# Kernel optimization log

Measured on AMD Instinct MI355X. Metric: run time of the kernel, lower is better.

## Reference

```python
import jax, jax.numpy as jnp
import numpy as np

B, S, HID = 1, 2048, 4096
N_HEADS, N_KV_HEADS, HEAD_DIM = 32, 8, 128
ROPE_THETA = 10000.0


def rotate_half(x):
    # standard Llama rotate_half along last dim
    d = x.shape[-1] // 2
    return jnp.concatenate([-x[..., d:], x[..., :d]], axis=-1)


def rope_cos_sin(position_ids, dtype):
    # inv_freq: [head_dim/2]
    inv_freq = 1.0 / (ROPE_THETA ** (jnp.arange(0, HEAD_DIM, 2, dtype=jnp.float32) / HEAD_DIM))
    freqs = position_ids.astype(jnp.float32)[:, :, None] * inv_freq[None, None, :]  # [B,S,hd/2]
    emb = jnp.concatenate([freqs, freqs], axis=-1)  # [B,S,hd]
    return jnp.cos(emb).astype(dtype), jnp.sin(emb).astype(dtype)


def setup_inputs() -> dict:
    key = jax.random.key(0)
    ks = jax.random.split(key, 5)
    scale = 0.02
    return {
        "hidden_states": jax.random.normal(ks[0], (B, S, HID), dtype=jnp.float32),
        "position_ids": jnp.broadcast_to(jnp.arange(S, dtype=jnp.int32)[None, :], (B, S)),
        "Wq": jax.random.normal(ks[1], (N_HEADS * HEAD_DIM, HID), dtype=jnp.float32) * scale,
        "Wk": jax.random.normal(ks[2], (N_KV_HEADS * HEAD_DIM, HID), dtype=jnp.float32) * scale,
        "Wv": jax.random.normal(ks[3], (N_KV_HEADS * HEAD_DIM, HID), dtype=jnp.float32) * scale,
        "Wo": jax.random.normal(ks[4], (HID, HID), dtype=jnp.float32) * scale,
    }


def reference(hidden_states, position_ids, Wq, Wk, Wv, Wo):
    bsz, q_len, _ = hidden_states.shape
    n_rep = N_HEADS // N_KV_HEADS

    # projections (torch Linear: x @ W.T)
    q = (hidden_states @ Wq.T).reshape(bsz, q_len, N_HEADS, HEAD_DIM).transpose(0, 2, 1, 3)
    k = (hidden_states @ Wk.T).reshape(bsz, q_len, N_KV_HEADS, HEAD_DIM).transpose(0, 2, 1, 3)
    v = (hidden_states @ Wv.T).reshape(bsz, q_len, N_KV_HEADS, HEAD_DIM).transpose(0, 2, 1, 3)

    cos, sin = rope_cos_sin(position_ids, hidden_states.dtype)
    cos = cos[:, None, :, :]  # [B,1,S,hd]
    sin = sin[:, None, :, :]
    q = q * cos + rotate_half(q) * sin
    k = k * cos + rotate_half(k) * sin

    # GQA: repeat kv heads
    k = jnp.repeat(k, n_rep, axis=1)  # [B,nH,S,hd]
    v = jnp.repeat(v, n_rep, axis=1)

    scores = jnp.einsum("bhqd,bhkd->bhqk", q, k) / jnp.sqrt(jnp.asarray(HEAD_DIM, q.dtype))
    causal = jnp.tril(jnp.ones((q_len, q_len), dtype=bool))
    neg = jnp.asarray(jnp.finfo(jnp.float32).min, scores.dtype)
    scores = jnp.where(causal[None, None, :, :], scores, neg)

    attn = jax.nn.softmax(scores.astype(jnp.float32), axis=-1).astype(q.dtype)
    out = jnp.einsum("bhqk,bhkd->bhqd", attn, v)  # [B,nH,S,hd]
    out = out.transpose(0, 2, 1, 3).reshape(bsz, q_len, HID)
    return out @ Wo.T
```

## Files before the change

### kernel.cpp

```cpp
#include <hip/hip_runtime.h>

typedef __attribute__((ext_vector_type(4))) float f32x4;
typedef __attribute__((ext_vector_type(8))) __bf16 bf16x8;
typedef __attribute__((ext_vector_type(4))) unsigned short u16x4;

#define DEVI static __device__ __forceinline__
#define AS1 __attribute__((address_space(1)))
#define AS3 __attribute__((address_space(3)))

static constexpr int S_LEN = 2048;
static constexpr int HID   = 4096;
static constexpr int NH    = 32;
static constexpr int NKV   = 8;
static constexpr int HD    = 128;
static constexpr int NQKV  = HID + 2 * NKV * HD;

DEVI unsigned short f2bf(float f) {
  unsigned int u = __float_as_uint(f);
  u += 0x7FFFu + ((u >> 16) & 1u);
  return (unsigned short)(u >> 16);
}
DEVI float bf2f(unsigned short h) {
  return __uint_as_float(((unsigned int)h) << 16);
}

__global__ void cast_f32_bf16(const float* __restrict__ in,
                              unsigned short* __restrict__ out, int n4) {
  int i = blockIdx.x * 256 + threadIdx.x;
  if (i >= n4) return;
  float4 v = reinterpret_cast<const float4*>(in)[i];
  u16x4 o;
  o[0] = f2bf(v.x); o[1] = f2bf(v.y); o[2] = f2bf(v.z); o[3] = f2bf(v.w);
  reinterpret_cast<u16x4*>(out)[i] = o;
}

__global__ void rope_table(float2* __restrict__ tab) {
  int i = blockIdx.x * 256 + threadIdx.x;
  if (i >= S_LEN * 64) return;
  int j = i & 63, s = i >> 6;
  float inv = powf(10000.0f, -(float)j / 64.0f);
  float ang = (float)s * inv;
  tab[i] = make_float2(cosf(ang), sinf(ang));
}

__global__ void rope_all(unsigned short* __restrict__ Qb,
                         unsigned short* __restrict__ Kb,
                         const float2* __restrict__ tab) {
  const int totq = S_LEN * NH * 64;
  const int tot  = totq + S_LEN * NKV * 64;
  int i = blockIdx.x * 256 + threadIdx.x;
  if (i >= tot) return;
  unsigned short* X; int Hn, idx;
  if (i < totq) { X = Qb; Hn = NH; idx = i; }
  else          { X = Kb; Hn = NKV; idx = i - totq; }
  int j = idx & 63;
  int h = (idx >> 6) % Hn;
  int s = idx / (64 * Hn);
  float2 cs = tab[s * 64 + j];
  unsigned short* p = X + (size_t)s * Hn * HD + h * HD;
  float x1 = bf2f(p[j]);
  float x2 = bf2f(p[j + 64]);
  p[j]      = f2bf(x1 * cs.x - x2 * cs.y);
  p[j + 64] = f2bf(x2 * cs.x + x1 * cs.y);
}

__global__ __launch_bounds__(512, 4) void gemm_qkv192(
    const unsigned short* __restrict__ A,
    const unsigned short* __restrict__ B,
    unsigned short* __restrict__ Qb,
    unsigned short* __restrict__ Kb,
    unsigned short* __restrict__ Vt) {
  __shared__ __align__(16) unsigned short lds[2][20480];
  const int tid = threadIdx.x;
  const int lane = tid & 63, w = tid >> 6;
  const int wm = w >> 2, wn = w & 3;
  const int lr = lane & 15, lg = lane >> 4;
  const int n0 = blockIdx.x * 192, m0 = blockIdx.y * 128;
  const int Kd = HID;

  const int sAr = tid >> 3, sAp = tid & 7;
  auto stA = [&](int buf, int t, int u) {
    int row = u * 64 + sAr;
    __builtin_amdgcn_global_load_lds(
        (const AS1 void*)(A + (size_t)(m0 + row) * Kd + t * 64 + ((sAp ^ (row & 7)) * 8)),
        (AS3 void*)(&lds[buf][row * 64 + sAp * 8]), 16, 0, 0);
  };
  auto stB = [&](int buf, int t, int v) {
    int row = v * 64 + sAr;
    __builtin_amdgcn_global_load_lds(
        (const AS1 void*)(B + (size_t)(n0 + row) * Kd + t * 64 + ((sAp ^ (row & 7)) * 8)),
        (AS3 void*)(&lds[buf][8192 + row * 64 + sAp * 8]), 16, 0, 0);
  };

  const int arow = (wm * 64 + lr) * 64;
  const int brow = 8192 + (wn * 48 + lr) * 64;
  const int ck0 = ((lg) ^ (lr & 7)) * 8;
  const int ck1 = ((4 + lg) ^ (lr & 7)) * 8;

  f32x4 acc[4][3] = {};
  bf16x8 bgr[3];

#pragma unroll
  for (int u = 0; u < 2; ++u) { stA(0, 0, u); stA(1, 1, u); }
#pragma unroll
  for (int v = 0; v < 3; ++v) { stB(0, 0, v); stB(1, 1, v); }
  asm volatile("s_waitcnt vmcnt(0)" ::: "memory");
  __builtin_amdgcn_s_barrier();

#define QPHASE(BUF, KH, MH, LOADB, WAITOP, ...)                                \
  do {                                                                         \
    const int ck = (KH) ? ck1 : ck0;                                           \
    const unsigned short* ab = &lds[BUF][arow + (MH) * 2048 + ck];             \
    bf16x8 af0 = *reinterpret_cast<const bf16x8*>(ab);                         \
    bf16x8 af1 = *reinterpret_cast<const bf16x8*>(ab + 1024);                  \
    if (LOADB) {                                                               \
      const unsigned short* bb = &lds[BUF][brow + ck];                         \
      bgr[0] = *reinterpret_cast<const bf16x8*>(bb);                           \
      bgr[1] = *reinterpret_cast<const bf16x8*>(bb + 1024);                    \
      bgr[2] = *reinterpret_cast<const bf16x8*>(bb + 2048);                    \
    }                                                                          \
    __builtin_amdgcn_sched_barrier(0);                                         \
    __VA_ARGS__                                                                \
    WAITOP                                                                     \
    __builtin_amdgcn_s_barrier();                                              \
    asm volatile("s_waitcnt lgkmcnt(0)" ::: "memory");                         \
    __builtin_amdgcn_sched_barrier(0);                                         \
    __builtin_amdgcn_s_setprio(1);                                             \
    acc[(MH)*2+0][0] = __builtin_amdgcn_mfma_f32_16x16x32_bf16(af0, bgr[0], acc[(MH)*2+0][0],0,0,0); \
    acc[(MH)*2+0][1] = __builtin_amdgcn_mfma_f32_16x16x32_bf16(af0, bgr[1], acc[(MH)*2+0][1],0,0,0); \
    acc[(MH)*2+0][2] = __builtin_amdgcn_mfma_f32_16x16x32_bf16(af0, bgr[2], acc[(MH)*2+0][2],0,0,0); \
    acc[(MH)*2+1][0] = __builtin_amdgcn_mfma_f32_16x16x32_bf16(af1, bgr[0], acc[(MH)*2+1][0],0,0,0); \
    acc[(MH)*2+1][1] = __builtin_amdgcn_mfma_f32_16x16x32_bf16(af1, bgr[1], acc[(MH)*2+1][1],0,0,0); \
    acc[(MH)*2+1][2] = __builtin_amdgcn_mfma_f32_16x16x32_bf16(af1, bgr[2], acc[(MH)*2+1][2],0,0,0); \
    __builtin_amdgcn_s_setprio(0);                                             \
    __builtin_amdgcn_s_barrier();                                              \
  } while (0)

#define QVM0 asm volatile("s_waitcnt vmcnt(0)" ::: "memory");
#define QNOW

  for (int i = 0; i < 32; ++i) {
    const int t = 2 * i;
    const bool nf = (i != 0), nl = (i != 31);
    QPHASE(0, 0, 0, 1, QNOW, if (nf) { stA(1, t + 1, 0); stA(1, t + 1, 1);
                                       stB(1, t + 1, 0); stB(1, t + 1, 1); stB(1, t + 1, 2); });
    QPHASE(0, 0, 1, 0, QNOW, ;);
    QPHASE(0, 1, 0, 1, QNOW, ;);
    QPHASE(0, 1, 1, 0, QVM0, ;);
    QPHASE(1, 0, 0, 1, QNOW, if (nl) { stA(0, t + 2, 0); stA(0, t + 2, 1);
                                       stB(0, t + 2, 0); stB(0, t + 2, 1); stB(0, t + 2, 2); });
    QPHASE(1, 0, 1, 0, QNOW, ;);
    QPHASE(1, 1, 0, 1, QNOW, ;);
    QPHASE(1, 1, 1, 0, QVM0, ;);
  }
#undef QPHASE
#undef QVM0
#undef QNOW

#pragma unroll
  for (int ar = 0; ar < 4; ++ar) {
#pragma unroll
    for (int c = 0; c < 3; ++c) {
      const int gcolb = n0 + wn * 48 + c * 16;
      const int gcol = gcolb + lr;
      const int growb = m0 + wm * 64 + ar * 16 + lg * 4;
      if (gcolb < HID) {
#pragma unroll
        for (int rr = 0; rr < 4; ++rr)
          Qb[(size_t)(growb + rr) * HID + gcol] = f2bf(acc[ar][c][rr]);
      } else if (gcolb < HID + NKV * HD) {
#pragma unroll
        for (int rr = 0; rr < 4; ++rr)
          Kb[(size_t)(growb + rr) * (NKV * HD) + (gcol - HID)] = f2bf(acc[ar][c][rr]);
      } else {
        u16x4 o4;
#pragma unroll
        for (int rr = 0; rr < 4; ++rr) o4[rr] = f2bf(acc[ar][c][rr]);
        *reinterpret_cast<u16x4*>(
            &Vt[(size_t)(gcol - HID - NKV * HD) * S_LEN + growb]) = o4;
      }
    }
  }
}

__global__ __launch_bounds__(512, 2) void gemm_o256(
    const unsigned short* __restrict__ A,
    const unsigned short* __restrict__ B,
    float* __restrict__ C) {
  __shared__ __align__(16) unsigned short lds[2][24576];
  const int tid = threadIdx.x;
  const int lane = tid & 63, w = tid >> 6;
  const int wm = w >> 2, wn = w & 3;
  const int lr = lane & 15, lg = lane >> 4;
  const int m0 = blockIdx.y * 128, n0 = blockIdx.x * 256;
  const int Kd = HID;

  const int sAr = tid >> 3, sAp = tid & 7;
  const int sBn = tid >> 2, sBp = tid & 3;
  auto stA = [&](int buf, int t, int unit) {
    int row = unit * 64 + sAr;
    __builtin_amdgcn_global_load_lds(
        (const AS1 void*)(A + (size_t)(m0 + row) * Kd + t * 64 + ((sAp ^ (row & 7)) * 8)),
        (AS3 void*)(&lds[buf][row * 64 + sAp * 8]), 16, 0, 0);
  };
  auto stB = [&](int buf, int t, int kh, int hb) {
    int n = hb * 128 + sBn;
    __builtin_amdgcn_global_load_lds(
        (const AS1 void*)(B + (size_t)(n0 + n) * Kd + t * 64 + kh * 32 + ((sBp ^ ((n >> 1) & 3)) * 8)),
        (AS3 void*)(&lds[buf][8192 + kh * 8192 + n * 32 + sBp * 8]), 16, 0, 0);
  };

  const int aoffk0 = (wm * 64 + lr) * 64 + ((lg ^ (lr & 7)) * 8);
  const int aoffk1 = (wm * 64 + lr) * 64 + (((4 + lg) ^ (lr & 7)) * 8);
  const int boff   = 8192 + (wn * 64 + lr) * 32 + ((lg ^ ((lr >> 1) & 3)) * 8);

  f32x4 acc[4][4] = {};
  bf16x8 bgr[4];

#pragma unroll
  for (int u = 0; u < 2; ++u) { stA(0, 0, u); stA(1, 1, u); }
#pragma unroll
  for (int kh = 0; kh < 2; ++kh)
#pragma unroll
    for (int hb = 0; hb < 2; ++hb) { stB(0, 0, kh, hb); stB(1, 1, kh, hb); }
  asm volatile("s_waitcnt vmcnt(0)" ::: "memory");
  __builtin_amdgcn_s_barrier();

#define OPHASE(BUF, KH, MH, LOADB, WAITOP, ...)                                \
  do {                                                                         \
    const unsigned short* ab = &lds[BUF][((KH) ? aoffk1 : aoffk0) + (MH) * 2048];\
    bf16x8 af0 = *reinterpret_cast<const bf16x8*>(ab);                         \
    bf16x8 af1 = *reinterpret_cast<const bf16x8*>(ab + 1024);                  \
    if (LOADB) {                                                               \
      const unsigned short* bb = &lds[BUF][boff + (KH) * 8192];                \
      bgr[0] = *reinterpret_cast<const bf16x8*>(bb);                           \
      bgr[1] = *reinterpret_cast<const bf16x8*>(bb + 512);                     \
      bgr[2] = *reinterpret_cast<const bf16x8*>(bb + 1024);                    \
      bgr[3] = *reinterpret_cast<const bf16x8*>(bb + 1536);                    \
    }                                                                          \
    __builtin_amdgcn_sched_barrier(0);                                         \
    __VA_ARGS__                                                                \
    WAITOP                                                                     \
    __builtin_amdgcn_s_barrier();                                              \
    asm volatile("s_waitcnt lgkmcnt(0)" ::: "memory");                         \
    __builtin_amdgcn_sched_barrier(0);                                         \
    __builtin_amdgcn_s_setprio(1);                                             \
    acc[(MH)*2+0][0] = __builtin_amdgcn_mfma_f32_16x16x32_bf16(af0, bgr[0], acc[(MH)*2+0][0],0,0,0); \
    acc[(MH)*2+0][1] = __builtin_amdgcn_mfma_f32_16x16x32_bf16(af0, bgr[1], acc[(MH)*2+0][1],0,0,0); \
    acc[(MH)*2+0][2] = __builtin_amdgcn_mfma_f32_16x16x32_bf16(af0, bgr[2], acc[(MH)*2+0][2],0,0,0); \
    acc[(MH)*2+0][3] = __builtin_amdgcn_mfma_f32_16x16x32_bf16(af0, bgr[3], acc[(MH)*2+0][3],0,0,0); \
    acc[(MH)*2+1][0] = __builtin_amdgcn_mfma_f32_16x16x32_bf16(af1, bgr[0], acc[(MH)*2+1][0],0,0,0); \
    acc[(MH)*2+1][1] = __builtin_amdgcn_mfma_f32_16x16x32_bf16(af1, bgr[1], acc[(MH)*2+1][1],0,0,0); \
    acc[(MH)*2+1][2] = __builtin_amdgcn_mfma_f32_16x16x32_bf16(af1, bgr[2], acc[(MH)*2+1][2],0,0,0); \
    acc[(MH)*2+1][3] = __builtin_amdgcn_mfma_f32_16x16x32_bf16(af1, bgr[3], acc[(MH)*2+1][3],0,0,0); \
    __builtin_amdgcn_s_setprio(0);                                             \
    __builtin_amdgcn_s_barrier();                                              \
  } while (0)

#define VM2 asm volatile("s_waitcnt vmcnt(2)" ::: "memory");
#define VM0 asm volatile("s_waitcnt vmcnt(0)" ::: "memory");
#define NOW

  for (int i = 0; i < 31; ++i) {
    const int t = 2 * i;
    const bool nf = (i != 0);
    OPHASE(0, 0, 0, 1, NOW, if (nf) { stA(1, t + 1, 0); stA(1, t + 1, 1);
                                      stB(1, t + 1, 1, 0); stB(1, t + 1, 1, 1); });
    OPHASE(0, 0, 1, 0, NOW, ;);
    OPHASE(0, 1, 0, 1, NOW, { stB(0, t + 2, 0, 0); stB(0, t + 2, 0, 1); });
    OPHASE(0, 1, 1, 0, VM2, ;);
    OPHASE(1, 0, 0, 1, NOW, { stA(0, t + 2, 0); stA(0, t + 2, 1);
                              stB(0, t + 2, 1, 0); stB(0, t + 2, 1, 1); });
    OPHASE(1, 0, 1, 0, NOW, ;);
    OPHASE(1, 1, 0, 1, NOW, { stB(1, t + 3, 0, 0); stB(1, t + 3, 0, 1); });
    OPHASE(1, 1, 1, 0, VM2, ;);
  }
  {
    const int t = 62;
    OPHASE(0, 0, 0, 1, NOW, { stA(1, t + 1, 0); stA(1, t + 1, 1);
                              stB(1, t + 1, 1, 0); stB(1, t + 1, 1, 1); });
    OPHASE(0, 0, 1, 0, NOW, ;);
    OPHASE(0, 1, 0, 1, NOW, ;);
    OPHASE(0, 1, 1, 0, VM0, ;);
    OPHASE(1, 0, 0, 1, NOW, ;);
    OPHASE(1, 0, 1, 0, NOW, ;);
    OPHASE(1, 1, 0, 1, NOW, ;);
    OPHASE(1, 1, 1, 0, NOW, ;);
  }
#undef OPHASE
#undef VM2
#undef VM0
#undef NOW

#pragma unroll
  for (int ar = 0; ar < 4; ++ar) {
#pragma unroll
    for (int fc = 0; fc < 4; ++fc) {
      const int gcol = n0 + wn * 64 + fc * 16 + lr;
      const int growb = m0 + wm * 64 + ar * 16 + lg * 4;
#pragma unroll
      for (int rr = 0; rr < 4; ++rr)
        C[(size_t)(growb + rr) * HID + gcol] = acc[ar][fc][rr];
    }
  }
}

__global__ __launch_bounds__(512, 4) void attn_kernel(
    const unsigned short* __restrict__ Q,
    const unsigned short* __restrict__ Kb,
    const unsigned short* __restrict__ Vt,
    unsigned short* __restrict__ O) {
  __shared__ __align__(16) unsigned short sK[2][64 * 128];
  __shared__ __align__(16) unsigned short sV[2][128 * 64];
  const int tid = threadIdx.x;
  const int lane = tid & 63, w = tid >> 6;
  const int lr = lane & 15, lg = lane >> 4;
  const int b = blockIdx.x;
  const int half = b >> 8, u = b & 255;
  const int h = u & 31, kvh = (u & 31) >> 2;
  const int j = u >> 5;
  const int qt = half ? (15 - j) : j;
  const int q0 = qt * 128, qw = q0 + w * 16;
  const int KVS = NKV * HD;

  bf16x8 qf[4];
#pragma unroll
  for (int ks = 0; ks < 4; ++ks)
    qf[ks] = *reinterpret_cast<const bf16x8*>(
        &Q[(size_t)(qw + lr) * HID + h * HD + ks * 32 + lg * 8]);

  f32x4 ao[8] = {};
  float mrun = -INFINITY, lrun = 0.f;
  const float S2 = 0.12751745f;
  const int ntiles = 2 * qt + 2;

  auto stage = [&](int bb, int kv0) {
#pragma unroll
    for (int i = 0; i < 2; ++i) {
      int off = (tid + i * 512) * 8;
      int r = off >> 7, c = (off >> 3) & 15;
      __builtin_amdgcn_global_load_lds(
          (const AS1 void*)(Kb + (size_t)(kv0 + r) * KVS + kvh * HD + ((c ^ (r & 15)) * 8)),
          (AS3 void*)(&sK[bb][off]), 16, 0, 0);
    }
#pragma unroll
    for (int i = 0; i < 2; ++i) {
      int off = (tid + i * 512) * 8;
      int r = off >> 6, c = (off >> 3) & 7;
      __builtin_amdgcn_global_load_lds(
          (const AS1 void*)(Vt + (size_t)(kvh * HD + r) * S_LEN + kv0 + ((c ^ (r & 7)) * 8)),
          (AS3 void*)(&sV[bb][off]), 16, 0, 0);
    }
  };

  stage(0, 0);
  __syncthreads();
  int cur = 0;

  for (int t = 0; t < ntiles; ++t) {
    const int kv0 = t * 64;
    if (t + 1 < ntiles) stage(cur ^ 1, kv0 + 64);

    if (kv0 <= qw + 15) {
      f32x4 sacc[4] = {};
      __builtin_amdgcn_s_setprio(1);
#pragma unroll
      for (int kt = 0; kt < 4; ++kt)
#pragma unroll
        for (int ks = 0; ks < 4; ++ks) {
          int elem = (kt * 16 + lr) * 128 + (((4 * ks + lg) ^ lr) * 8);
          bf16x8 kf = *reinterpret_cast<const bf16x8*>(&sK[cur][elem]);
          sacc[kt] = __builtin_amdgcn_mfma_f32_16x16x32_bf16(kf, qf[ks], sacc[kt], 0, 0, 0);
        }
      __builtin_amdgcn_s_setprio(0);

      const bool needMask = (kv0 + 63 > qw);
      const int qg = qw + lr;
      float p[16];
      float tmax = -INFINITY;
#pragma unroll
      for (int kt = 0; kt < 4; ++kt)
#pragma unroll
        for (int r = 0; r < 4; ++r) {
          float v = sacc[kt][r] * S2;
          if (needMask && (kv0 + kt * 16 + lg * 4 + r > qg)) v = -INFINITY;
          p[kt * 4 + r] = v;
          tmax = fmaxf(tmax, v);
        }
      tmax = fmaxf(tmax, __shfl_xor(tmax, 16));
      tmax = fmaxf(tmax, __shfl_xor(tmax, 32));
      if (!__all(tmax <= mrun + 8.0f)) {
        float mnew = fmaxf(mrun, tmax);
        float corr = exp2f(mrun - mnew);
        lrun *= corr;
#pragma unroll
        for (int dt = 0; dt < 8; ++dt) ao[dt] *= corr;
        mrun = mnew;
      }
      float rs = 0.f;
#pragma unroll
      for (int i = 0; i < 16; ++i) { p[i] = exp2f(p[i] - mrun); rs += p[i]; }
      rs += __shfl_xor(rs, 16);
      rs += __shfl_xor(rs, 32);
      lrun += rs;

      unsigned int bfrag[2][4];
#pragma unroll
      for (int g = 0; g < 2; ++g) {
        unsigned int Au = (unsigned)f2bf(p[8 * g + 0]) | ((unsigned)f2bf(p[8 * g + 1]) << 16);
        unsigned int Bu = (unsigned)f2bf(p[8 * g + 2]) | ((unsigned)f2bf(p[8 * g + 3]) << 16);
        unsigned int Cu = (unsigned)f2bf(p[8 * g + 4]) | ((unsigned)f2bf(p[8 * g + 5]) << 16);
        unsigned int Du = (unsigned)f2bf(p[8 * g + 6]) | ((unsigned)f2bf(p[8 * g + 7]) << 16);
        int s0 = (lg & 1) * 2;
        int src0 = lr + 16 * s0, src1 = src0 + 16;
        bool hi = lg >= 2;
        int a0 = __shfl((int)Au, src0), c0 = __shfl((int)Cu, src0);
        int b0 = __shfl((int)Bu, src0), d0 = __shfl((int)Du, src0);
        int a1 = __shfl((int)Au, src1), c1 = __shfl((int)Cu, src1);
        int b1 = __shfl((int)Bu, src1), d1 = __shfl((int)Du, src1);
        bfrag[g][0] = hi ? (unsigned)c0 : (unsigned)a0;
        bfrag[g][1] = hi ? (unsigned)d0 : (unsigned)b0;
        bfrag[g][2] = hi ? (unsigned)c1 : (unsigned)a1;
        bfrag[g][3] = hi ? (unsigned)d1 : (unsigned)b1;
      }

      __builtin_amdgcn_s_setprio(1);
#pragma unroll
      for (int g = 0; g < 2; ++g)
#pragma unroll
        for (int dt = 0; dt < 8; ++dt) {
          int d = dt * 16 + lr;
          int elem = d * 64 + (((4 * g + lg) ^ (lr & 7)) * 8);
          bf16x8 vf = *reinterpret_cast<const bf16x8*>(&sV[cur][elem]);
          ao[dt] = __builtin_amdgcn_mfma_f32_16x16x32_bf16(
              vf, *reinterpret_cast<const bf16x8*>(&bfrag[g]), ao[dt], 0, 0, 0);
        }
      __builtin_amdgcn_s_setprio(0);
    }

    __syncthreads();
    cur ^= 1;
  }

  float inv = 1.0f / lrun;
  int qrow = qw + lr;
#pragma unroll
  for (int dt = 0; dt < 8; ++dt) {
    u16x4 o4;
#pragma unroll
    for (int r = 0; r < 4; ++r) o4[r] = f2bf(ao[dt][r] * inv);
    *reinterpret_cast<u16x4*>(&O[(size_t)qrow * HID + h * HD + dt * 16 + lg * 4]) = o4;
  }
}

extern "C" void kernel_launch(void* const* d_in, const int* in_sizes, int n_in,
                              void* d_out, int out_size, void* d_ws, size_t ws_size,
                              hipStream_t stream) {
  const float* hs = (const float*)d_in[0];
  const float* Wq = (const float*)d_in[2];
  const float* Wk = (const float*)d_in[3];
  const float* Wv = (const float*)d_in[4];
  const float* Wo = (const float*)d_in[5];

  unsigned short* ws = (unsigned short*)d_ws;
  size_t off = 0;
  unsigned short* H16  = ws + off; off += (size_t)S_LEN * HID;
  unsigned short* Wcat = ws + off; off += (size_t)NQKV * HID;
  unsigned short* Qb   = ws + off; off += (size_t)S_LEN * HID;
  unsigned short* Kb   = ws + off; off += (size_t)S_LEN * NKV * HD;
  unsigned short* Vt   = ws + off; off += (size_t)S_LEN * NKV * HD;
  float2* tab = (float2*)(ws + off); off += (size_t)S_LEN * 64 * 2 * 2;

  auto cast = [&](const float* src, unsigned short* dst, size_t n) {
    int n4 = (int)(n / 4);
    cast_f32_bf16<<<(n4 + 255) / 256, 256, 0, stream>>>(src, dst, n4);
  };

  rope_table<<<(S_LEN * 64 + 255) / 256, 256, 0, stream>>>(tab);
  cast(hs, H16, (size_t)S_LEN * HID);
  cast(Wq, Wcat, (size_t)HID * HID);
  cast(Wk, Wcat + (size_t)HID * HID, (size_t)NKV * HD * HID);
  cast(Wv, Wcat + (size_t)(HID + NKV * HD) * HID, (size_t)NKV * HD * HID);

  gemm_qkv192<<<dim3(NQKV / 192, S_LEN / 128), 512, 0, stream>>>(
      H16, Wcat, Qb, Kb, Vt);

  cast(Wo, Wcat, (size_t)HID * HID);

  {
    int tot = S_LEN * NH * 64 + S_LEN * NKV * 64;
    rope_all<<<(tot + 255) / 256, 256, 0, stream>>>(Qb, Kb, tab);
  }

  attn_kernel<<<dim3(512), 512, 0, stream>>>(Qb, Kb, Vt, H16);

  gemm_o256<<<dim3(HID / 256, S_LEN / 128), 512, 0, stream>>>(
      H16, Wcat, (float*)d_out);
}
```

Before: 323.2 us.

## Enlarge QKV GEMM tile to 256x192 and fuse input casts into one kernel

The QKV projection GEMM now uses a 256x192 block tile. Each of 8 waves computes a 64x96 sub-tile with 24 accumulators instead of 12, which doubles reuse of B fragments per LDS read and halves the grid in M. The four separate f32-to-bf16 cast launches for hidden states and Wq/Wk/Wv are merged into a single kernel to cut launch overhead. The larger tile raises register and LDS use (occupancy hint lowered to 2) and leaves fewer blocks for the CUs, which risks worse latency hiding and poorer load balance.

```diff
diff --git a/kernel.cpp b/kernel.cpp
--- a/kernel.cpp
+++ b/kernel.cpp
@@ -32,6 +32,28 @@
   u16x4 o;
   o[0] = f2bf(v.x); o[1] = f2bf(v.y); o[2] = f2bf(v.z); o[3] = f2bf(v.w);
   reinterpret_cast<u16x4*>(out)[i] = o;
+}
+
+__global__ void cast_all(const float* __restrict__ hs,
+                         const float* __restrict__ Wq,
+                         const float* __restrict__ Wk,
+                         const float* __restrict__ Wv,
+                         unsigned short* __restrict__ H16,
+                         unsigned short* __restrict__ Wcat) {
+  const int nH  = S_LEN * HID / 4;
+  const int nWq = HID * HID / 4;
+  const int nWkv = NKV * HD * HID / 4;
+  int i = blockIdx.x * 256 + threadIdx.x;
+  const float* src; unsigned short* dst; int idx;
+  if (i < nH)                    { src = hs; dst = H16; idx = i; }
+  else if (i < nH + nWq)         { src = Wq; dst = Wcat; idx = i - nH; }
+  else if (i < nH + nWq + nWkv)  { src = Wk; dst = Wcat + (size_t)HID * HID; idx = i - nH - nWq; }
+  else                           { src = Wv; dst = Wcat + (size_t)(HID + NKV * HD) * HID;
+                                   idx = i - nH - nWq - nWkv; }
+  float4 v = reinterpret_cast<const float4*>(src)[idx];
+  u16x4 o;
+  o[0] = f2bf(v.x); o[1] = f2bf(v.y); o[2] = f2bf(v.z); o[3] = f2bf(v.w);
+  reinterpret_cast<u16x4*>(dst)[idx] = o;
 }
 
 __global__ void rope_table(float2* __restrict__ tab) {
@@ -64,18 +86,18 @@
   p[j + 64] = f2bf(x2 * cs.x + x1 * cs.y);
 }
 
-__global__ __launch_bounds__(512, 4) void gemm_qkv192(
+__global__ __launch_bounds__(512, 2) void gemm_qkv96(
     const unsigned short* __restrict__ A,
     const unsigned short* __restrict__ B,
     unsigned short* __restrict__ Qb,
     unsigned short* __restrict__ Kb,
     unsigned short* __restrict__ Vt) {
-  __shared__ __align__(16) unsigned short lds[2][20480];
+  __shared__ __align__(16) unsigned short lds[2][28672];
   const int tid = threadIdx.x;
   const int lane = tid & 63, w = tid >> 6;
-  const int wm = w >> 2, wn = w & 3;
+  const int wm = w >> 1, wn = w & 1;
   const int lr = lane & 15, lg = lane >> 4;
-  const int n0 = blockIdx.x * 192, m0 = blockIdx.y * 128;
+  const int n0 = blockIdx.x * 192, m0 = blockIdx.y * 256;
   const int Kd = HID;
 
   const int sAr = tid >> 3, sAp = tid & 7;
@@ -89,19 +111,19 @@
     int row = v * 64 + sAr;
     __builtin_amdgcn_global_load_lds(
         (const AS1 void*)(B + (size_t)(n0 + row) * Kd + t * 64 + ((sAp ^ (row & 7)) * 8)),
-        (AS3 void*)(&lds[buf][8192 + row * 64 + sAp * 8]), 16, 0, 0);
+        (AS3 void*)(&lds[buf][16384 + row * 64 + sAp * 8]), 16, 0, 0);
   };
 
   const int arow = (wm * 64 + lr) * 64;
-  const int brow = 8192 + (wn * 48 + lr) * 64;
-  const int ck0 = ((lg) ^ (lr & 7)) * 8;
+  const int brow = 16384 + (wn * 96 + lr) * 64;
+  const int ck0 = (lg ^ (lr & 7)) * 8;
   const int ck1 = ((4 + lg) ^ (lr & 7)) * 8;
 
-  f32x4 acc[4][3] = {};
-  bf16x8 bgr[3];
-
-#pragma unroll
-  for (int u = 0; u < 2; ++u) { stA(0, 0, u); stA(1, 1, u); }
+  f32x4 acc[4][6] = {};
+  bf16x8 bgr[6];
+
+#pragma unroll
+  for (int u = 0; u < 4; ++u) { stA(0, 0, u); stA(1, 1, u); }
 #pragma unroll
   for (int v = 0; v < 3; ++v) { stB(0, 0, v); stB(1, 1, v); }
   asm volatile("s_waitcnt vmcnt(0)" ::: "memory");
@@ -118,6 +140,9 @@
       bgr[0] = *reinterpret_cast<const bf16x8*>(bb);                           \
       bgr[1] = *reinterpret_cast<const bf16x8*>(bb + 1024);                    \
       bgr[2] = *reinterpret_cast<const bf16x8*>(bb + 2048);                    \
+      bgr[3] = *reinterpret_cast<const bf16x8*>(bb + 3072);                    \
+      bgr[4] = *reinterpret_cast<const bf16x8*>(bb + 4096);                    \
+      bgr[5] = *reinterpret_cast<const bf16x8*>(bb + 5120);                    \
     }                                                                          \
     __builtin_amdgcn_sched_barrier(0);                                         \
     __VA_ARGS__                                                                \
@@ -129,9 +154,15 @@
     acc[(MH)*2+0][0] = __builtin_amdgcn_mfma_f32_16x16x32_bf16(af0, bgr[0], acc[(MH)*2+0][0],0,0,0); \
     acc[(MH)*2+0][1] = __builtin_amdgcn_mfma_f32_16x16x32_bf16(af0, bgr[1], acc[(MH)*2+0][1],0,0,0); \
     acc[(MH)*2+0][2] = __builtin_amdgcn_mfma_f32_16x16x32_bf16(af0, bgr[2], acc[(MH)*2+0][2],0,0,0); \
+    acc[(MH)*2+0][3] = __builtin_amdgcn_mfma_f32_16x16x32_bf16(af0, bgr[3], acc[(MH)*2+0][3],0,0,0); \
+    acc[(MH)*2+0][4] = __builtin_amdgcn_mfma_f32_16x16x32_bf16(af0, bgr[4], acc[(MH)*2+0][4],0,0,0); \
+    acc[(MH)*2+0][5] = __builtin_amdgcn_mfma_f32_16x16x32_bf16(af0, bgr[5], acc[(MH)*2+0][5],0,0,0); \
     acc[(MH)*2+1][0] = __builtin_amdgcn_mfma_f32_16x16x32_bf16(af1, bgr[0], acc[(MH)*2+1][0],0,0,0); \
     acc[(MH)*2+1][1] = __builtin_amdgcn_mfma_f32_16x16x32_bf16(af1, bgr[1], acc[(MH)*2+1][1],0,0,0); \
     acc[(MH)*2+1][2] = __builtin_amdgcn_mfma_f32_16x16x32_bf16(af1, bgr[2], acc[(MH)*2+1][2],0,0,0); \
+    acc[(MH)*2+1][3] = __builtin_amdgcn_mfma_f32_16x16x32_bf16(af1, bgr[3], acc[(MH)*2+1][3],0,0,0); \
+    acc[(MH)*2+1][4] = __builtin_amdgcn_mfma_f32_16x16x32_bf16(af1, bgr[4], acc[(MH)*2+1][4],0,0,0); \
+    acc[(MH)*2+1][5] = __builtin_amdgcn_mfma_f32_16x16x32_bf16(af1, bgr[5], acc[(MH)*2+1][5],0,0,0); \
     __builtin_amdgcn_s_setprio(0);                                             \
     __builtin_amdgcn_s_barrier();                                              \
   } while (0)
@@ -143,11 +174,13 @@
     const int t = 2 * i;
     const bool nf = (i != 0), nl = (i != 31);
     QPHASE(0, 0, 0, 1, QNOW, if (nf) { stA(1, t + 1, 0); stA(1, t + 1, 1);
+                                       stA(1, t + 1, 2); stA(1, t + 1, 3);
                                        stB(1, t + 1, 0); stB(1, t + 1, 1); stB(1, t + 1, 2); });
     QPHASE(0, 0, 1, 0, QNOW, ;);
     QPHASE(0, 1, 0, 1, QNOW, ;);
     QPHASE(0, 1, 1, 0, QVM0, ;);
     QPHASE(1, 0, 0, 1, QNOW, if (nl) { stA(0, t + 2, 0); stA(0, t + 2, 1);
+                                       stA(0, t + 2, 2); stA(0, t + 2, 3);
                                        stB(0, t + 2, 0); stB(0, t + 2, 1); stB(0, t + 2, 2); });
     QPHASE(1, 0, 1, 0, QNOW, ;);
     QPHASE(1, 1, 0, 1, QNOW, ;);
@@ -160,8 +193,8 @@
 #pragma unroll
   for (int ar = 0; ar < 4; ++ar) {
 #pragma unroll
-    for (int c = 0; c < 3; ++c) {
-      const int gcolb = n0 + wn * 48 + c * 16;
+    for (int c = 0; c < 6; ++c) {
+      const int gcolb = n0 + wn * 96 + c * 16;
       const int gcol = gcolb + lr;
       const int growb = m0 + wm * 64 + ar * 16 + lg * 4;
       if (gcolb < HID) {
@@ -471,21 +504,20 @@
   unsigned short* Vt   = ws + off; off += (size_t)S_LEN * NKV * HD;
   float2* tab = (float2*)(ws + off); off += (size_t)S_LEN * 64 * 2 * 2;
 
-  auto cast = [&](const float* src, unsigned short* dst, size_t n) {
-    int n4 = (int)(n / 4);
-    cast_f32_bf16<<<(n4 + 255) / 256, 256, 0, stream>>>(src, dst, n4);
-  };
-
   rope_table<<<(S_LEN * 64 + 255) / 256, 256, 0, stream>>>(tab);
-  cast(hs, H16, (size_t)S_LEN * HID);
-  cast(Wq, Wcat, (size_t)HID * HID);
-  cast(Wk, Wcat + (size_t)HID * HID, (size_t)NKV * HD * HID);
-  cast(Wv, Wcat + (size_t)(HID + NKV * HD) * HID, (size_t)NKV * HD * HID);
-
-  gemm_qkv192<<<dim3(NQKV / 192, S_LEN / 128), 512, 0, stream>>>(
+
+  {
+    int n4 = (S_LEN * HID + HID * HID + 2 * NKV * HD * HID) / 4;
+    cast_all<<<(n4 + 255) / 256, 256, 0, stream>>>(hs, Wq, Wk, Wv, H16, Wcat);
+  }
+
+  gemm_qkv96<<<dim3(NQKV / 192, S_LEN / 256), 512, 0, stream>>>(
       H16, Wcat, Qb, Kb, Vt);
 
-  cast(Wo, Wcat, (size_t)HID * HID);
+  {
+    int n4 = HID * HID / 4;
+    cast_f32_bf16<<<(n4 + 255) / 256, 256, 0, stream>>>(Wo, Wcat, n4);
+  }
 
   {
     int tot = S_LEN * NH * 64 + S_LEN * NKV * 64;
```

After: 314.7 us. 2.6% less time.
